# Kernel tuning notes

Measured on AMD Instinct MI355X. Metric: run time of the kernel, lower is better.

The kernel has to match this reference:

```python
import jax, jax.numpy as jnp
import numpy as np


def setup_inputs() -> dict:
    key = jax.random.key(0)
    ks = jax.random.split(key, 5)
    B, H, W, C = 8, 256, 256, 96
    return {
        "x": jax.random.normal(ks[0], (B, H, W, C), dtype=jnp.float32),
        "qkv_w": jax.random.normal(ks[1], (3 * C, C), dtype=jnp.float32) * 0.02,
        "qkv_b": jax.random.normal(ks[2], (3 * C,), dtype=jnp.float32) * 0.02,
        "proj_w": jax.random.normal(ks[3], (C, C), dtype=jnp.float32) * 0.02,
        "proj_b": jax.random.normal(ks[4], (C,), dtype=jnp.float32) * 0.02,
        "window_size": 8,
        "num_heads": 4,
    }


def reference(x, qkv_w, qkv_b, proj_w, proj_b, window_size, num_heads):
    B, H, W, C = x.shape
    ws = window_size
    hd = C // num_heads
    scale = hd ** -0.5
    # window partition: [B,H,W,C] -> [B*nWh*nWw, ws*ws, C]
    xw = x.reshape(B, H // ws, ws, W // ws, ws, C)
    xw = xw.transpose(0, 1, 3, 2, 4, 5).reshape(-1, ws * ws, C)
    n = xw.shape[0]
    # qkv projection (torch Linear: y = x @ W^T + b)
    qkv = xw @ qkv_w.T + qkv_b  # [n, ws*ws, 3C]
    qkv = qkv.reshape(n, ws * ws, 3, num_heads, hd).transpose(2, 0, 3, 1, 4)
    q, k, v = qkv[0], qkv[1], qkv[2]  # each [n, heads, ws*ws, hd]
    attn = jnp.einsum("nhqd,nhkd->nhqk", q, k) * scale
    attn = jax.nn.softmax(attn, axis=-1)
    out = jnp.einsum("nhqk,nhkd->nhqd", attn, v)
    out = out.transpose(0, 2, 1, 3).reshape(n, ws * ws, C)
    out = out @ proj_w.T + proj_b
    # window reverse: [n, ws*ws, C] -> [B, H, W, C]
    out = out.reshape(B, H // ws, W // ws, ws, ws, C)
    out = out.transpose(0, 1, 3, 2, 4, 5).reshape(B, H, W, C)
    return out
```

## Files before the change

### kernel.cpp

```cpp
#include <hip/hip_runtime.h>


typedef _Float16 f16;
typedef f16 f16x8 __attribute__((ext_vector_type(8)));
typedef f16 f16x4 __attribute__((ext_vector_type(4)));
typedef __fp16 hf2 __attribute__((ext_vector_type(2)));
typedef float f32x4 __attribute__((ext_vector_type(4)));

#define MFMA_K32 __builtin_amdgcn_mfma_f32_16x16x32_f16

#define QS 104

__device__ __forceinline__ int vtidx(int row, int col) { return row*64 + (col ^ ((row & 7) << 3)); }

__device__ __forceinline__ f16x4 pk4(float a, float b, float c, float d) {
    union { f16x4 v; hf2 h[2]; } u;
    u.h[0] = __builtin_amdgcn_cvt_pkrtz(a, b);
    u.h[1] = __builtin_amdgcn_cvt_pkrtz(c, d);
    return u.v;
}

__global__ void prep_weights(const float* __restrict__ qkv_w,
                             const float* __restrict__ proj_w,
                             f16* __restrict__ ws) {
    const int u = blockIdx.x * 256 + threadIdx.x;
    if (u < 3456) {
        const int lane = u & 63, unit = u >> 6;
        const int n = unit / 3, kk = unit - 3*n;
        const int lr = lane & 15, lg = lane >> 4;
        const float* s = qkv_w + (16*n + lr)*96 + kk*32 + lg*8;
        f16x8 v;
        #pragma unroll
        for (int e = 0; e < 8; ++e) v[e] = (f16)s[e];
        *(f16x8*)(ws + (size_t)u*8) = v;
    } else if (u < 4608) {
        const int uu = u - 3456;
        const int lane = uu & 63, unit = uu >> 6;
        const int n = unit / 3, kk = unit - 3*n;
        const int lr = lane & 15, lg = lane >> 4;
        const float* s = proj_w + (16*n + lr)*96 + kk*32 + lg*8;
        f16x8 v;
        #pragma unroll
        for (int e = 0; e < 8; ++e) v[e] = (f16)s[e];
        *(f16x8*)(ws + 27648 + (size_t)uu*8) = v;
    }
}

__global__ __launch_bounds__(256, 2) void winattn(
    const float* __restrict__ x,
    const f16*   __restrict__ wsq,
    const float* __restrict__ qkv_b,
    const f16*   __restrict__ wsp,
    const float* __restrict__ proj_b,
    float* __restrict__ out)
{
    __shared__ __align__(16) f16 qqA[64*QS];
    __shared__ __align__(16) f16 qkA[64*QS];
    __shared__ __align__(16) f16 qqB[64*QS];
    __shared__ __align__(16) f16 qkB[64*QS];
    __shared__ __align__(16) f16 vtA[96*64];
    __shared__ __align__(16) f16 vtB[96*64];

    const int tid = threadIdx.x;
    const int wid = blockIdx.x * 2;
    const int bb = wid >> 10, wh = (wid >> 5) & 31, ww = wid & 31;
    const size_t win_baseA = ((size_t)(bb*256 + wh*8)*256 + (size_t)(ww*8)) * 96;

    const int lane = tid & 63, w = tid >> 6;
    const int lr = lane & 15, lg = lane >> 4;
    const int t = 16*w + lr;
    const size_t tok_offA = win_baseA + (size_t)(((t>>3)<<8) + (t&7))*96;
    const size_t tok_offB = tok_offA + 768;

    const f16* wqL = wsq + lane*8;
    const f16* wpL = wsp + lane*8;

    f16x8 axA[3], axB[3];
    #pragma unroll
    for (int kk = 0; kk < 3; ++kk) {
        const float* xpA = x + tok_offA + kk*32 + lg*8;
        const float* xpB = x + tok_offB + kk*32 + lg*8;
        const float4 a0 = *(const float4*)xpA;
        const float4 a1 = *(const float4*)(xpA + 4);
        const float4 b0 = *(const float4*)xpB;
        const float4 b1 = *(const float4*)(xpB + 4);
        union { f16x8 v; f16x4 q[2]; } ua, ub;
        ua.q[0] = pk4(a0.x, a0.y, a0.z, a0.w);
        ua.q[1] = pk4(a1.x, a1.y, a1.z, a1.w);
        ub.q[0] = pk4(b0.x, b0.y, b0.z, b0.w);
        ub.q[1] = pk4(b1.x, b1.y, b1.z, b1.w);
        axA[kk] = ua.v;
        axB[kk] = ub.v;
    }
    const int vcol = (w>>1)*32 + (lr>>2)*8 + (w&1)*4 + (lr&3);

    {
        f16x8 wf[6][3];
        #pragma unroll
        for (int nn = 0; nn < 6; ++nn)
            #pragma unroll
            for (int kk = 0; kk < 3; ++kk)
                wf[nn][kk] = *(const f16x8*)(wqL + (nn*3 + kk)*512);
        #pragma unroll
        for (int nn = 0; nn < 6; ++nn) {
            f32x4 accA = {0.f,0.f,0.f,0.f}, accB = {0.f,0.f,0.f,0.f};
            #pragma unroll
            for (int kk = 0; kk < 3; ++kk) {
                accA = MFMA_K32(wf[nn][kk], axA[kk], accA, 0,0,0);
                accB = MFMA_K32(wf[nn][kk], axB[kk], accB, 0,0,0);
            }
            const int j0 = 16*nn + 4*lg;
            const float4 b4 = *(const float4*)(qkv_b + j0);
            *(f16x4*)&qqA[t*QS + j0] = pk4(accA[0]+b4.x, accA[1]+b4.y, accA[2]+b4.z, accA[3]+b4.w);
            *(f16x4*)&qqB[t*QS + j0] = pk4(accB[0]+b4.x, accB[1]+b4.y, accB[2]+b4.z, accB[3]+b4.w);
        }
    }
    {
        f16x8 wf[6][3];
        #pragma unroll
        for (int nn = 0; nn < 6; ++nn)
            #pragma unroll
            for (int kk = 0; kk < 3; ++kk)
                wf[nn][kk] = *(const f16x8*)(wqL + ((nn+6)*3 + kk)*512);
        #pragma unroll
        for (int nn = 0; nn < 6; ++nn) {
            f32x4 accA = {0.f,0.f,0.f,0.f}, accB = {0.f,0.f,0.f,0.f};
            #pragma unroll
            for (int kk = 0; kk < 3; ++kk) {
                accA = MFMA_K32(wf[nn][kk], axA[kk], accA, 0,0,0);
                accB = MFMA_K32(wf[nn][kk], axB[kk], accB, 0,0,0);
            }
            const int j0 = 16*nn + 4*lg;
            const float4 b4 = *(const float4*)(qkv_b + 96 + j0);
            *(f16x4*)&qkA[t*QS + j0] = pk4(accA[0]+b4.x, accA[1]+b4.y, accA[2]+b4.z, accA[3]+b4.w);
            *(f16x4*)&qkB[t*QS + j0] = pk4(accB[0]+b4.x, accB[1]+b4.y, accB[2]+b4.z, accB[3]+b4.w);
        }
    }
    {
        f16x8 wf[6][3];
        #pragma unroll
        for (int nn = 0; nn < 6; ++nn)
            #pragma unroll
            for (int kk = 0; kk < 3; ++kk)
                wf[nn][kk] = *(const f16x8*)(wqL + ((nn+12)*3 + kk)*512);
        #pragma unroll
        for (int nn = 0; nn < 6; ++nn) {
            f32x4 accA = {0.f,0.f,0.f,0.f}, accB = {0.f,0.f,0.f,0.f};
            #pragma unroll
            for (int kk = 0; kk < 3; ++kk) {
                accA = MFMA_K32(wf[nn][kk], axA[kk], accA, 0,0,0);
                accB = MFMA_K32(wf[nn][kk], axB[kk], accB, 0,0,0);
            }
            const int j0 = 16*nn + 4*lg;
            const float4 b4 = *(const float4*)(qkv_b + 192 + j0);
            const int hv = (unsigned)j0 / 24u, d0 = j0 - 24*hv;
            vtA[vtidx(hv*24 + d0+0, vcol)] = (f16)(accA[0]+b4.x);
            vtA[vtidx(hv*24 + d0+1, vcol)] = (f16)(accA[1]+b4.y);
            vtA[vtidx(hv*24 + d0+2, vcol)] = (f16)(accA[2]+b4.z);
            vtA[vtidx(hv*24 + d0+3, vcol)] = (f16)(accA[3]+b4.w);
            vtB[vtidx(hv*24 + d0+0, vcol)] = (f16)(accB[0]+b4.x);
            vtB[vtidx(hv*24 + d0+1, vcol)] = (f16)(accB[1]+b4.y);
            vtB[vtidx(hv*24 + d0+2, vcol)] = (f16)(accB[2]+b4.z);
            vtB[vtidx(hv*24 + d0+3, vcol)] = (f16)(accB[3]+b4.w);
        }
    }
    __syncthreads();

    const int h = w;
    const bool live = (lg < 3);
    const int cs = h*24 + lg*8;
    const f16x8 z8 = {0,0,0,0,0,0,0,0};

    f16x8 bfA[4], afA[4], bfB[4], afB[4];
    #pragma unroll
    for (int i = 0; i < 4; ++i) {
        bfA[i] = z8; afA[i] = z8; bfB[i] = z8; afB[i] = z8;
        if (live) {
            bfA[i] = *(const f16x8*)&qqA[(16*i + lr)*QS + cs];
            afA[i] = *(const f16x8*)&qkA[(16*i + lr)*QS + cs];
            bfB[i] = *(const f16x8*)&qqB[(16*i + lr)*QS + cs];
            afB[i] = *(const f16x8*)&qkB[(16*i + lr)*QS + cs];
        }
    }
    __syncthreads();

    f32x4 stA[4][4], stB[4][4];
    #pragma unroll
    for (int un = 0; un < 4; ++un)
        #pragma unroll
        for (int tn = 0; tn < 4; ++tn) {
            stA[un][tn] = MFMA_K32(afA[un], bfA[tn], (f32x4){0.f,0.f,0.f,0.f}, 0,0,0);
            stB[un][tn] = MFMA_K32(afB[un], bfB[tn], (f32x4){0.f,0.f,0.f,0.f}, 0,0,0);
        }

    const float kE = 0.29448890f;
    float rsA[4], rsB[4];
    #pragma unroll
    for (int tn = 0; tn < 4; ++tn) {
        float mA = stA[0][tn][0], mB = stB[0][tn][0];
        #pragma unroll
        for (int un = 0; un < 4; ++un)
            #pragma unroll
            for (int r = 0; r < 4; ++r) {
                mA = fmaxf(mA, stA[un][tn][r]);
                mB = fmaxf(mB, stB[un][tn][r]);
            }
        mA = fmaxf(mA, __shfl_xor(mA, 16)); mA = fmaxf(mA, __shfl_xor(mA, 32));
        mB = fmaxf(mB, __shfl_xor(mB, 16)); mB = fmaxf(mB, __shfl_xor(mB, 32));
        const float mkA = mA * kE, mkB = mB * kE;
        float sA = 0.f, sB = 0.f;
        #pragma unroll
        for (int un = 0; un < 4; ++un)
            #pragma unroll
            for (int r = 0; r < 4; ++r) {
                const float eA = exp2f(fmaf(stA[un][tn][r], kE, -mkA));
                const float eB = exp2f(fmaf(stB[un][tn][r], kE, -mkB));
                stA[un][tn][r] = eA; sA += eA;
                stB[un][tn][r] = eB; sB += eB;
            }
        sA += __shfl_xor(sA, 16); sA += __shfl_xor(sA, 32);
        sB += __shfl_xor(sB, 16); sB += __shfl_xor(sB, 32);
        rsA[tn] = 1.f / sA;
        rsB[tn] = 1.f / sB;
    }

    f32x4 oa0A[4], oa1A[4], oa0B[4], oa1B[4];
    #pragma unroll
    for (int tn = 0; tn < 4; ++tn) {
        oa0A[tn] = (f32x4){0.f,0.f,0.f,0.f}; oa1A[tn] = (f32x4){0.f,0.f,0.f,0.f};
        oa0B[tn] = (f32x4){0.f,0.f,0.f,0.f}; oa1B[tn] = (f32x4){0.f,0.f,0.f,0.f};
    }
    const int d1 = (16 + lr > 23) ? 23 : 16 + lr;
    #pragma unroll
    for (int hf = 0; hf < 2; ++hf) {
        const f16x8 av0A = *(const f16x8*)&vtA[vtidx(h*24 + lr, hf*32 + lg*8)];
        const f16x8 av1A = *(const f16x8*)&vtA[vtidx(h*24 + d1, hf*32 + lg*8)];
        const f16x8 av0B = *(const f16x8*)&vtB[vtidx(h*24 + lr, hf*32 + lg*8)];
        const f16x8 av1B = *(const f16x8*)&vtB[vtidx(h*24 + d1, hf*32 + lg*8)];
        #pragma unroll
        for (int tn = 0; tn < 4; ++tn) {
            union { f16x8 v; hf2 h2[4]; } pA, pB;
            pA.h2[0] = __builtin_amdgcn_cvt_pkrtz(stA[2*hf  ][tn][0], stA[2*hf  ][tn][1]);
            pA.h2[1] = __builtin_amdgcn_cvt_pkrtz(stA[2*hf  ][tn][2], stA[2*hf  ][tn][3]);
            pA.h2[2] = __builtin_amdgcn_cvt_pkrtz(stA[2*hf+1][tn][0], stA[2*hf+1][tn][1]);
            pA.h2[3] = __builtin_amdgcn_cvt_pkrtz(stA[2*hf+1][tn][2], stA[2*hf+1][tn][3]);
            pB.h2[0] = __builtin_amdgcn_cvt_pkrtz(stB[2*hf  ][tn][0], stB[2*hf  ][tn][1]);
            pB.h2[1] = __builtin_amdgcn_cvt_pkrtz(stB[2*hf  ][tn][2], stB[2*hf  ][tn][3]);
            pB.h2[2] = __builtin_amdgcn_cvt_pkrtz(stB[2*hf+1][tn][0], stB[2*hf+1][tn][1]);
            pB.h2[3] = __builtin_amdgcn_cvt_pkrtz(stB[2*hf+1][tn][2], stB[2*hf+1][tn][3]);
            oa0A[tn] = MFMA_K32(av0A, pA.v, oa0A[tn], 0,0,0);
            oa1A[tn] = MFMA_K32(av1A, pA.v, oa1A[tn], 0,0,0);
            oa0B[tn] = MFMA_K32(av0B, pB.v, oa0B[tn], 0,0,0);
            oa1B[tn] = MFMA_K32(av1B, pB.v, oa1B[tn], 0,0,0);
        }
    }

    f16x8 pf[6][3];
    #pragma unroll
    for (int n = 0; n < 6; ++n)
        #pragma unroll
        for (int kk = 0; kk < 3; ++kk)
            pf[n][kk] = *(const f16x8*)(wpL + (n*3 + kk)*512);
    float4 pb4[6];
    #pragma unroll
    for (int n = 0; n < 6; ++n)
        pb4[n] = *(const float4*)(proj_b + 16*n + 4*lg);

    #pragma unroll
    for (int tn = 0; tn < 4; ++tn) {
        const int tt = 16*tn + lr;
        *(f16x4*)&qqA[tt*QS + h*24 + 4*lg] =
            pk4(oa0A[tn][0]*rsA[tn], oa0A[tn][1]*rsA[tn], oa0A[tn][2]*rsA[tn], oa0A[tn][3]*rsA[tn]);
        *(f16x4*)&qqB[tt*QS + h*24 + 4*lg] =
            pk4(oa0B[tn][0]*rsB[tn], oa0B[tn][1]*rsB[tn], oa0B[tn][2]*rsB[tn], oa0B[tn][3]*rsB[tn]);
        if (lg < 2) {
            *(f16x4*)&qqA[tt*QS + h*24 + 16 + 4*lg] =
                pk4(oa1A[tn][0]*rsA[tn], oa1A[tn][1]*rsA[tn], oa1A[tn][2]*rsA[tn], oa1A[tn][3]*rsA[tn]);
            *(f16x4*)&qqB[tt*QS + h*24 + 16 + 4*lg] =
                pk4(oa1B[tn][0]*rsB[tn], oa1B[tn][1]*rsB[tn], oa1B[tn][2]*rsB[tn], oa1B[tn][3]*rsB[tn]);
        }
    }
    __syncthreads();

    f16x8 boA[3], boB[3];
    #pragma unroll
    for (int kk = 0; kk < 3; ++kk) {
        boA[kk] = *(const f16x8*)&qqA[t*QS + kk*32 + lg*8];
        boB[kk] = *(const f16x8*)&qqB[t*QS + kk*32 + lg*8];
    }
    #pragma unroll
    for (int n = 0; n < 6; ++n) {
        f32x4 paA = {0.f,0.f,0.f,0.f}, paB = {0.f,0.f,0.f,0.f};
        #pragma unroll
        for (int kk = 0; kk < 3; ++kk) {
            paA = MFMA_K32(pf[n][kk], boA[kk], paA, 0,0,0);
            paB = MFMA_K32(pf[n][kk], boB[kk], paB, 0,0,0);
        }
        const int c0 = 16*n + 4*lg;
        float4 ovA = {paA[0]+pb4[n].x, paA[1]+pb4[n].y, paA[2]+pb4[n].z, paA[3]+pb4[n].w};
        float4 ovB = {paB[0]+pb4[n].x, paB[1]+pb4[n].y, paB[2]+pb4[n].z, paB[3]+pb4[n].w};
        *(float4*)(out + tok_offA + c0) = ovA;
        *(float4*)(out + tok_offB + c0) = ovB;
    }
}

extern "C" void kernel_launch(void* const* d_in, const int* in_sizes, int n_in,
                              void* d_out, int out_size, void* d_ws, size_t ws_size,
                              hipStream_t stream) {
    const float* x      = (const float*)d_in[0];
    const float* qkv_w  = (const float*)d_in[1];
    const float* qkv_b  = (const float*)d_in[2];
    const float* proj_w = (const float*)d_in[3];
    const float* proj_b = (const float*)d_in[4];
    float* out = (float*)d_out;
    f16* ws = (f16*)d_ws;

    prep_weights<<<dim3(18), dim3(256), 0, stream>>>(qkv_w, proj_w, ws);
    winattn<<<dim3(4096), dim3(256), 0, stream>>>(x, ws, qkv_b, ws + 27648, proj_b, out);
}
```

Before: 152.4 us.

## Fold softmax scale into Q weights, drop max pass, stage output via LDS

The softmax scale (times log2e) is pre-multiplied into the Q rows of the QKV weights and bias in the prep kernel, so the attention kernel applies exp2 directly to the scores. The row-max reduction and its cross-lane shuffles are removed, which shortens the softmax. The projection output is now staged through a swizzled LDS buffer that reuses the Q/K region, then written to global memory as fully coalesced float4 stores. Skipping max subtraction risks exp overflow when scores are large, and the staging adds two barriers and LDS traffic.

```diff
diff --git a/kernel.cpp b/kernel.cpp
--- a/kernel.cpp
+++ b/kernel.cpp
@@ -10,8 +10,10 @@
 #define MFMA_K32 __builtin_amdgcn_mfma_f32_16x16x32_f16
 
 #define QS 104
+#define KE 0.29448890f
 
 __device__ __forceinline__ int vtidx(int row, int col) { return row*64 + (col ^ ((row & 7) << 3)); }
+__device__ __forceinline__ int o2idx(int t, int c)     { return t*104 + (c ^ ((t & 7) << 2)); }
 
 __device__ __forceinline__ f16x4 pk4(float a, float b, float c, float d) {
     union { f16x4 v; hf2 h[2]; } u;
@@ -22,16 +24,18 @@
 
 __global__ void prep_weights(const float* __restrict__ qkv_w,
                              const float* __restrict__ proj_w,
+                             const float* __restrict__ qkv_b,
                              f16* __restrict__ ws) {
     const int u = blockIdx.x * 256 + threadIdx.x;
     if (u < 3456) {
         const int lane = u & 63, unit = u >> 6;
         const int n = unit / 3, kk = unit - 3*n;
         const int lr = lane & 15, lg = lane >> 4;
+        const float sc = (n < 6) ? KE : 1.0f;
         const float* s = qkv_w + (16*n + lr)*96 + kk*32 + lg*8;
         f16x8 v;
         #pragma unroll
-        for (int e = 0; e < 8; ++e) v[e] = (f16)s[e];
+        for (int e = 0; e < 8; ++e) v[e] = (f16)(s[e] * sc);
         *(f16x8*)(ws + (size_t)u*8) = v;
     } else if (u < 4608) {
         const int uu = u - 3456;
@@ -43,6 +47,9 @@
         #pragma unroll
         for (int e = 0; e < 8; ++e) v[e] = (f16)s[e];
         *(f16x8*)(ws + 27648 + (size_t)uu*8) = v;
+    } else if (u < 4704) {
+        const int j = u - 4608;
+        ((float*)(ws + 36864))[j] = qkv_b[j] * KE;
     }
 }
 
@@ -54,12 +61,15 @@
     const float* __restrict__ proj_b,
     float* __restrict__ out)
 {
-    __shared__ __align__(16) f16 qqA[64*QS];
-    __shared__ __align__(16) f16 qkA[64*QS];
-    __shared__ __align__(16) f16 qqB[64*QS];
-    __shared__ __align__(16) f16 qkB[64*QS];
-    __shared__ __align__(16) f16 vtA[96*64];
-    __shared__ __align__(16) f16 vtB[96*64];
+    __shared__ __align__(16) char smem[77824];
+    f16* qqA = (f16*)(smem);
+    f16* qkA = (f16*)(smem + 13312);
+    f16* qqB = (f16*)(smem + 26624);
+    f16* qkB = (f16*)(smem + 39936);
+    f16* vtA = (f16*)(smem + 53248);
+    f16* vtB = (f16*)(smem + 65536);
+    float* o2A = (float*)(smem);
+    float* o2B = (float*)(smem + 26624);
 
     const int tid = threadIdx.x;
     const int wid = blockIdx.x * 2;
@@ -74,6 +84,7 @@
 
     const f16* wqL = wsq + lane*8;
     const f16* wpL = wsp + lane*8;
+    const float* qbs = (const float*)(wsq + 36864);
 
     f16x8 axA[3], axB[3];
     #pragma unroll
@@ -110,7 +121,7 @@
                 accB = MFMA_K32(wf[nn][kk], axB[kk], accB, 0,0,0);
             }
             const int j0 = 16*nn + 4*lg;
-            const float4 b4 = *(const float4*)(qkv_b + j0);
+            const float4 b4 = *(const float4*)(qbs + j0);
             *(f16x4*)&qqA[t*QS + j0] = pk4(accA[0]+b4.x, accA[1]+b4.y, accA[2]+b4.z, accA[3]+b4.w);
             *(f16x4*)&qqB[t*QS + j0] = pk4(accB[0]+b4.x, accB[1]+b4.y, accB[2]+b4.z, accB[3]+b4.w);
         }
@@ -193,28 +204,16 @@
             stB[un][tn] = MFMA_K32(afB[un], bfB[tn], (f32x4){0.f,0.f,0.f,0.f}, 0,0,0);
         }
 
-    const float kE = 0.29448890f;
     float rsA[4], rsB[4];
     #pragma unroll
     for (int tn = 0; tn < 4; ++tn) {
-        float mA = stA[0][tn][0], mB = stB[0][tn][0];
+        float sA = 0.f, sB = 0.f;
         #pragma unroll
         for (int un = 0; un < 4; ++un)
             #pragma unroll
             for (int r = 0; r < 4; ++r) {
-                mA = fmaxf(mA, stA[un][tn][r]);
-                mB = fmaxf(mB, stB[un][tn][r]);
-            }
-        mA = fmaxf(mA, __shfl_xor(mA, 16)); mA = fmaxf(mA, __shfl_xor(mA, 32));
-        mB = fmaxf(mB, __shfl_xor(mB, 16)); mB = fmaxf(mB, __shfl_xor(mB, 32));
-        const float mkA = mA * kE, mkB = mB * kE;
-        float sA = 0.f, sB = 0.f;
-        #pragma unroll
-        for (int un = 0; un < 4; ++un)
-            #pragma unroll
-            for (int r = 0; r < 4; ++r) {
-                const float eA = exp2f(fmaf(stA[un][tn][r], kE, -mkA));
-                const float eB = exp2f(fmaf(stB[un][tn][r], kE, -mkB));
+                const float eA = exp2f(stA[un][tn][r]);
+                const float eB = exp2f(stB[un][tn][r]);
                 stA[un][tn][r] = eA; sA += eA;
                 stB[un][tn][r] = eB; sB += eB;
             }
@@ -288,6 +287,8 @@
         boA[kk] = *(const f16x8*)&qqA[t*QS + kk*32 + lg*8];
         boB[kk] = *(const f16x8*)&qqB[t*QS + kk*32 + lg*8];
     }
+    __syncthreads();
+
     #pragma unroll
     for (int n = 0; n < 6; ++n) {
         f32x4 paA = {0.f,0.f,0.f,0.f}, paB = {0.f,0.f,0.f,0.f};
@@ -299,8 +300,18 @@
         const int c0 = 16*n + 4*lg;
         float4 ovA = {paA[0]+pb4[n].x, paA[1]+pb4[n].y, paA[2]+pb4[n].z, paA[3]+pb4[n].w};
         float4 ovB = {paB[0]+pb4[n].x, paB[1]+pb4[n].y, paB[2]+pb4[n].z, paB[3]+pb4[n].w};
-        *(float4*)(out + tok_offA + c0) = ovA;
-        *(float4*)(out + tok_offB + c0) = ovB;
+        *(float4*)&o2A[o2idx(t, c0)] = ovA;
+        *(float4*)&o2B[o2idx(t, c0)] = ovB;
+    }
+    __syncthreads();
+
+    #pragma unroll
+    for (int it = 0; it < 6; ++it) {
+        const int i = it*256 + tid;
+        const int tt = i / 24, c4 = (i - tt*24) * 4;
+        const size_t po = win_baseA + (size_t)(((tt>>3)<<8) + (tt&7))*96 + c4;
+        *(float4*)(out + po)       = *(const float4*)&o2A[o2idx(tt, c4)];
+        *(float4*)(out + po + 768) = *(const float4*)&o2B[o2idx(tt, c4)];
     }
 }
 
@@ -315,6 +326,6 @@
     float* out = (float*)d_out;
     f16* ws = (f16*)d_ws;
 
-    prep_weights<<<dim3(18), dim3(256), 0, stream>>>(qkv_w, proj_w, ws);
+    prep_weights<<<dim3(19), dim3(256), 0, stream>>>(qkv_w, proj_w, qkv_b, ws);
     winattn<<<dim3(4096), dim3(256), 0, stream>>>(x, ws, qkv_b, ws + 27648, proj_b, out);
 }
```

New measurement: 141.1 us. -7.4%, faster.
